# Kernel optimization log

Measured on AMD Instinct MI355X. Metric: run time of the kernel, lower is better.

The kernel has to match this reference:

```python
import jax, jax.numpy as jnp
import numpy as np

H = 64          # HIDDEN_DIM
VOCAB = 64      # VOCAB_SIZE
B, L = 256, 512
LN_EPS = 1e-5
NORM_EPS = 1e-12  # F.normalize eps


def setup_inputs() -> dict:
    key = jax.random.key(0)
    ks = jax.random.split(key, 12)
    s = 0.05
    return {
        "seq": jax.random.randint(ks[0], (B, L), 0, VOCAB),
        "embed": jax.random.normal(ks[1], (VOCAB, H), jnp.float32),
        "w1": jax.random.normal(ks[2], (H, 2 * H), jnp.float32) * s,
        "b1": jnp.zeros((2 * H,), jnp.float32),
        "w2": jax.random.normal(ks[3], (2 * H, H), jnp.float32) * s,
        "b2": jnp.zeros((H,), jnp.float32),
        "ln_g": jnp.ones((H,), jnp.float32),
        "ln_b": jnp.zeros((H,), jnp.float32),
        "rp_w": jax.random.normal(ks[4], (H, H), jnp.float32) * s,
        "rp_b": jnp.zeros((H,), jnp.float32),
        "out_w": jax.random.normal(ks[5], (H, VOCAB), jnp.float32) * s,
        "out_b": jnp.zeros((VOCAB,), jnp.float32),
    }


def reference(seq, embed, w1, b1, w2, b2, ln_g, ln_b, rp_w, rp_b, out_w, out_b):
    h = embed[seq]                                   # [B, L, H]
    ff = jnp.maximum(h @ w1 + b1, 0.0) @ w2 + b2     # MLP with ReLU
    x = h + ff
    mu = x.mean(-1, keepdims=True)
    var = x.var(-1, keepdims=True)                   # population variance (torch LN)
    h = (x - mu) / jnp.sqrt(var + LN_EPS) * ln_g + ln_b

    b, l, hd = h.shape
    ks = jnp.swapaxes(h, 0, 1)[:-1]                  # [L-1, B, H] keys over time

    def step(M, k):
        # k: [B, H]; M: [B, H, H] fast-weight memory
        kn = k / jnp.maximum(jnp.linalg.norm(k, axis=-1, keepdims=True), NORM_EPS)
        vp = jnp.einsum('bij,bj->bi', M, kn)         # predicted value
        dv = k - vp                                  # delta-rule error
        M = M + jnp.einsum('bi,bj->bij', dv, kn)     # alpha=1.0 -> full update
        return M, None

    M0 = jnp.zeros((b, hd, hd), h.dtype)
    M, _ = jax.lax.scan(step, M0, ks)

    y = jnp.einsum('bij,bj->bi', M, h[:, -1, :])     # read with last token
    return (y @ rp_w + rp_b) @ out_w + out_b         # [B, VOCAB]
```

## Files before the change

### kernel.cpp

```cpp
#include <hip/hip_runtime.h>

#define SEQLEN 512
#define NBATCH 256

typedef __attribute__((ext_vector_type(8))) __bf16 bf16x8;
typedef __attribute__((ext_vector_type(4))) float f32x4;
typedef unsigned short u16;
typedef unsigned int u32;

union B8 { bf16x8 v; u16 s[8]; uint4 q; };

__device__ __forceinline__ u16 rneb(float f) {
    u32 u = __float_as_uint(f);
    return (u16)((u + 0x7FFFu + ((u >> 16) & 1u)) >> 16);
}

template <int CTRL>
__device__ __forceinline__ float dpp_add(float x) {
    int y = __builtin_amdgcn_update_dpp(0, __float_as_int(x), CTRL, 0xF, 0xF, true);
    return x + __int_as_float(y);
}
__device__ __forceinline__ float sum16(float x) {
    x = dpp_add<0xB1>(x);
    x = dpp_add<0x4E>(x);
    x = dpp_add<0x141>(x);
    x = dpp_add<0x140>(x);
    return x;
}

__global__ __launch_bounds__(256, 1) void fused_all(
    const int* __restrict__ seq, const float* __restrict__ embed,
    const float* __restrict__ w1, const float* __restrict__ b1,
    const float* __restrict__ w2, const float* __restrict__ b2,
    const float* __restrict__ ln_g, const float* __restrict__ ln_b,
    const float* __restrict__ rp_w, const float* __restrict__ rp_b,
    const float* __restrict__ out_w, const float* __restrict__ out_b,
    float* __restrict__ out)
{
    __shared__ __align__(16) unsigned char smem[149504];
    float* Ksh = (float*)smem;
    float* Ssh = (float*)(smem + 131072);
    u16*  t1b  = (u16*)(smem + 133120);
    float* ysh = (float*)(smem + 133120);
    float* zsh = ysh + 64;

    const int tid = threadIdx.x;
    const int wv  = tid >> 6;
    const int l   = tid & 63;
    const int g   = l >> 4;
    const int tl  = l & 15;
    const int b   = blockIdx.x;

    B8 wA0[8], wA1[8];
#pragma unroll
    for (int nt = 0; nt < 8; ++nt) {
        const int j = nt * 16 + tl;
#pragma unroll
        for (int e = 0; e < 8; ++e) {
            wA0[nt].s[e] = rneb(w1[(g * 8 + e) * 128 + j]);
            wA1[nt].s[e] = rneb(w1[(32 + g * 8 + e) * 128 + j]);
        }
    }
    B8 wB[4][4];
#pragma unroll
    for (int kk = 0; kk < 4; ++kk)
#pragma unroll
        for (int mt = 0; mt < 4; ++mt) {
            const int m = mt * 16 + tl;
#pragma unroll
            for (int e = 0; e < 8; ++e)
                wB[kk][mt].s[e] = rneb(w2[(kk * 32 + g * 8 + e) * 64 + m]);
        }

    u16* myT = t1b + wv * 2048 + tl * 128;
    const int swz = (tl & 7) << 3;

    for (int grp = 0; grp < 8; ++grp) {
        const int lt = wv * 128 + grp * 16 + tl;
        const int idx = seq[b * SEQLEN + lt];
        const float* erow = embed + idx * 64;

        B8 xb0, xb1;
        {
            float4 c0 = *reinterpret_cast<const float4*>(erow + g * 8);
            float4 c1 = *reinterpret_cast<const float4*>(erow + g * 8 + 4);
            xb0.s[0] = rneb(c0.x); xb0.s[1] = rneb(c0.y); xb0.s[2] = rneb(c0.z); xb0.s[3] = rneb(c0.w);
            xb0.s[4] = rneb(c1.x); xb0.s[5] = rneb(c1.y); xb0.s[6] = rneb(c1.z); xb0.s[7] = rneb(c1.w);
            float4 c2 = *reinterpret_cast<const float4*>(erow + 32 + g * 8);
            float4 c3 = *reinterpret_cast<const float4*>(erow + 32 + g * 8 + 4);
            xb1.s[0] = rneb(c2.x); xb1.s[1] = rneb(c2.y); xb1.s[2] = rneb(c2.z); xb1.s[3] = rneb(c2.w);
            xb1.s[4] = rneb(c3.x); xb1.s[5] = rneb(c3.y); xb1.s[6] = rneb(c3.z); xb1.s[7] = rneb(c3.w);
        }

        f32x4 acc[8];
#pragma unroll
        for (int nt = 0; nt < 8; ++nt) acc[nt] = (f32x4){0.f, 0.f, 0.f, 0.f};
#pragma unroll
        for (int nt = 0; nt < 8; ++nt) {
            acc[nt] = __builtin_amdgcn_mfma_f32_16x16x32_bf16(wA0[nt].v, xb0.v, acc[nt], 0, 0, 0);
            acc[nt] = __builtin_amdgcn_mfma_f32_16x16x32_bf16(wA1[nt].v, xb1.v, acc[nt], 0, 0, 0);
        }

#pragma unroll
        for (int nt = 0; nt < 8; ++nt) {
            float4 bb = *reinterpret_cast<const float4*>(b1 + nt * 16 + g * 4);
            u32 lo = (u32)rneb(fmaxf(acc[nt][0] + bb.x, 0.f)) |
                     ((u32)rneb(fmaxf(acc[nt][1] + bb.y, 0.f)) << 16);
            u32 hi = (u32)rneb(fmaxf(acc[nt][2] + bb.z, 0.f)) |
                     ((u32)rneb(fmaxf(acc[nt][3] + bb.w, 0.f)) << 16);
            *reinterpret_cast<uint2*>(&myT[(nt * 16 + g * 4) ^ swz]) = make_uint2(lo, hi);
        }

        f32x4 acc2[4];
#pragma unroll
        for (int mt = 0; mt < 4; ++mt) acc2[mt] = (f32x4){0.f, 0.f, 0.f, 0.f};
#pragma unroll
        for (int kk = 0; kk < 4; ++kk) {
            B8 tb; tb.q = *reinterpret_cast<const uint4*>(&myT[(kk * 32 + g * 8) ^ swz]);
#pragma unroll
            for (int mt = 0; mt < 4; ++mt)
                acc2[mt] = __builtin_amdgcn_mfma_f32_16x16x32_bf16(wB[kk][mt].v, tb.v, acc2[mt], 0, 0, 0);
        }

        float x[16];
        float sum = 0.f;
#pragma unroll
        for (int mt = 0; mt < 4; ++mt) {
            float4 hr  = *reinterpret_cast<const float4*>(erow + mt * 16 + g * 4);
            float4 b2v = *reinterpret_cast<const float4*>(b2 + mt * 16 + g * 4);
            x[4*mt+0] = acc2[mt][0] + hr.x + b2v.x;
            x[4*mt+1] = acc2[mt][1] + hr.y + b2v.y;
            x[4*mt+2] = acc2[mt][2] + hr.z + b2v.z;
            x[4*mt+3] = acc2[mt][3] + hr.w + b2v.w;
            sum += x[4*mt+0] + x[4*mt+1] + x[4*mt+2] + x[4*mt+3];
        }
        sum += __shfl_xor(sum, 16);
        sum += __shfl_xor(sum, 32);
        float mu = sum * (1.f / 64.f);

        float vs = 0.f;
#pragma unroll
        for (int i = 0; i < 16; ++i) { float d = x[i] - mu; vs = fmaf(d, d, vs); }
        vs += __shfl_xor(vs, 16);
        vs += __shfl_xor(vs, 32);
        float rstd = 1.f / sqrtf(vs * (1.f / 64.f) + 1e-5f);

        float ss = 0.f;
#pragma unroll
        for (int mt = 0; mt < 4; ++mt) {
            float4 gv = *reinterpret_cast<const float4*>(ln_g + mt * 16 + g * 4);
            float4 bv = *reinterpret_cast<const float4*>(ln_b + mt * 16 + g * 4);
            float k0 = fmaf((x[4*mt+0] - mu) * rstd, gv.x, bv.x);
            float k1 = fmaf((x[4*mt+1] - mu) * rstd, gv.y, bv.y);
            float k2 = fmaf((x[4*mt+2] - mu) * rstd, gv.z, bv.z);
            float k3 = fmaf((x[4*mt+3] - mu) * rstd, gv.w, bv.w);
            x[4*mt+0] = k0; x[4*mt+1] = k1; x[4*mt+2] = k2; x[4*mt+3] = k3;
            ss = fmaf(k0, k0, ss); ss = fmaf(k1, k1, ss);
            ss = fmaf(k2, k2, ss); ss = fmaf(k3, k3, ss);
        }
        ss += __shfl_xor(ss, 16);
        ss += __shfl_xor(ss, 32);
        float s = fmaxf(sqrtf(ss), 1e-12f);
        float rn = 1.f / s;

        const int rsw = (lt & 7) << 3;
#pragma unroll
        for (int mt = 0; mt < 4; ++mt)
            *reinterpret_cast<float4*>(Ksh + lt * 64 + ((mt * 16 + g * 4) ^ rsw)) =
                make_float4(x[4*mt+0] * rn, x[4*mt+1] * rn, x[4*mt+2] * rn, x[4*mt+3] * rn);
        if (l < 16) Ssh[lt] = s;
    }

    __syncthreads();

    if (wv == 0) {
        const int c16 = l & 15;

        float4 qi = *reinterpret_cast<const float4*>(Ksh + 511 * 64 + ((c16 * 4) ^ 56));
        float s511 = Ssh[511];
        float u0 = qi.x * s511, u1 = qi.y * s511, u2 = qi.z * s511, u3 = qi.w * s511;
        float y0 = 0.f, y1 = 0.f, y2 = 0.f, y3 = 0.f;

        auto step = [&](float4 kf, float st) {
            float p = fmaf(kf.x, u0, kf.y * u1) + fmaf(kf.z, u2, kf.w * u3);
            float c_ = sum16(p);
            float cs = c_ * st;
            u0 = fmaf(-c_, kf.x, u0); u1 = fmaf(-c_, kf.y, u1);
            u2 = fmaf(-c_, kf.z, u2); u3 = fmaf(-c_, kf.w, u3);
            y0 = fmaf(cs, kf.x, y0); y1 = fmaf(cs, kf.y, y1);
            y2 = fmaf(cs, kf.z, y2); y3 = fmaf(cs, kf.w, y3);
        };

#define KLOADL(KA, SA, CH) do {                                               \
    _Pragma("unroll")                                                         \
    for (int q = 0; q < 8; ++q) {                                             \
        int trow = 510 - 8 * (CH) - q;                                        \
        int cr = trow < 0 ? 0 : trow;                                         \
        KA[q] = *reinterpret_cast<const float4*>(                             \
            Ksh + cr * 64 + ((c16 * 4) ^ ((cr & 7) << 3)));                   \
        SA[q] = Ssh[cr];                                                      \
    } } while (0)

        float4 bA[8], bB[8];
        float  sA[8], sB[8];
        KLOADL(bA, sA, 0);
        KLOADL(bB, sB, 1);
        for (int c = 0; c < 62; c += 2) {
#pragma unroll
            for (int q = 0; q < 8; ++q) step(bA[q], sA[q]);
            KLOADL(bA, sA, c + 2);
#pragma unroll
            for (int q = 0; q < 8; ++q) step(bB[q], sB[q]);
            KLOADL(bB, sB, c + 3);
        }
#pragma unroll
        for (int q = 0; q < 8; ++q) step(bA[q], sA[q]);
#pragma unroll
        for (int q = 0; q < 7; ++q) step(bB[q], sB[q]);

        if (l < 16)
            *reinterpret_cast<float4*>(&ysh[c16 * 4]) = make_float4(y0, y1, y2, y3);
    }
    __syncthreads();

    float z = 0.f;
    if (tid < 64) {
        z = rp_b[tid];
#pragma unroll 8
        for (int j = 0; j < 64; ++j) z = fmaf(ysh[j], rp_w[j * 64 + tid], z);
    }
    __syncthreads();
    if (tid < 64) zsh[tid] = z;
    __syncthreads();
    if (tid < 64) {
        float o = out_b[tid];
#pragma unroll 8
        for (int j = 0; j < 64; ++j) o = fmaf(zsh[j], out_w[j * 64 + tid], o);
        out[b * 64 + tid] = o;
    }
}

extern "C" void kernel_launch(void* const* d_in, const int* in_sizes, int n_in,
                              void* d_out, int out_size, void* d_ws, size_t ws_size,
                              hipStream_t stream) {
    const int*   seq   = (const int*)d_in[0];
    const float* embed = (const float*)d_in[1];
    const float* w1    = (const float*)d_in[2];
    const float* b1    = (const float*)d_in[3];
    const float* w2    = (const float*)d_in[4];
    const float* b2    = (const float*)d_in[5];
    const float* ln_g  = (const float*)d_in[6];
    const float* ln_b  = (const float*)d_in[7];
    const float* rp_w  = (const float*)d_in[8];
    const float* rp_b  = (const float*)d_in[9];
    const float* out_w = (const float*)d_in[10];
    const float* out_b = (const float*)d_in[11];
    float* out = (float*)d_out;

    fused_all<<<NBATCH, 256, 0, stream>>>(seq, embed, w1, b1, w2, b2,
                                          ln_g, ln_b, rp_w, rp_b,
                                          out_w, out_b, out);
}
```

Measured before the change: 128.1 us.

## Block the delta-rule backward scan by four keys using precomputed Gram dot products

The serial dual-form recurrence now processes four keys per step. Pairwise dot products within each group of four are precomputed in parallel by all waves into shared memory, which turns four dependent cross-lane reductions into four independent ones followed by a small triangular solve. The block grows to 512 threads, and the MLP phase is split into halves to lower register pressure, which also shrinks the scratch buffer per wave. Launch bounds now request 2 blocks per CU, but the roughly 147 KB of static shared memory probably keeps it at one. The serial tail also drops a barrier and only wave 0 touches ysh/zsh.

Result: slower. 131.7 us (+2.8%).

```diff
diff --git a/kernel.cpp b/kernel.cpp
--- a/kernel.cpp
+++ b/kernel.cpp
@@ -28,7 +28,13 @@
     return x;
 }
 
-__global__ __launch_bounds__(256, 1) void fused_all(
+__device__ __forceinline__ float dot4(const float4& k, float u0, float u1,
+                                      float u2, float u3) {
+    return fmaf(k.x, u0, k.y * u1) + fmaf(k.z, u2, k.w * u3);
+}
+
+
+__global__ __launch_bounds__(512, 2) void fused_all(
     const int* __restrict__ seq, const float* __restrict__ embed,
     const float* __restrict__ w1, const float* __restrict__ b1,
     const float* __restrict__ w2, const float* __restrict__ b2,
@@ -41,8 +47,9 @@
     float* Ksh = (float*)smem;
     float* Ssh = (float*)(smem + 131072);
     u16*  t1b  = (u16*)(smem + 133120);
-    float* ysh = (float*)(smem + 133120);
-    float* zsh = ysh + 64;
+    float* Gq  = (float*)(smem + 133120);
+    float* ysh = (float*)(smem + 137216);
+    float* zsh = (float*)(smem + 137472);
 
     const int tid = threadIdx.x;
     const int wv  = tid >> 6;
@@ -72,11 +79,11 @@
                 wB[kk][mt].s[e] = rneb(w2[(kk * 32 + g * 8 + e) * 64 + m]);
         }
 
-    u16* myT = t1b + wv * 2048 + tl * 128;
+    u16* myT = t1b + wv * 1024 + tl * 64;
     const int swz = (tl & 7) << 3;
 
-    for (int grp = 0; grp < 8; ++grp) {
-        const int lt = wv * 128 + grp * 16 + tl;
+    for (int grp = 0; grp < 4; ++grp) {
+        const int lt = wv * 64 + grp * 16 + tl;
         const int idx = seq[b * SEQLEN + lt];
         const float* erow = embed + idx * 64;
 
@@ -92,34 +99,38 @@
             xb1.s[4] = rneb(c3.x); xb1.s[5] = rneb(c3.y); xb1.s[6] = rneb(c3.z); xb1.s[7] = rneb(c3.w);
         }
 
-        f32x4 acc[8];
-#pragma unroll
-        for (int nt = 0; nt < 8; ++nt) acc[nt] = (f32x4){0.f, 0.f, 0.f, 0.f};
-#pragma unroll
-        for (int nt = 0; nt < 8; ++nt) {
-            acc[nt] = __builtin_amdgcn_mfma_f32_16x16x32_bf16(wA0[nt].v, xb0.v, acc[nt], 0, 0, 0);
-            acc[nt] = __builtin_amdgcn_mfma_f32_16x16x32_bf16(wA1[nt].v, xb1.v, acc[nt], 0, 0, 0);
-        }
-
-#pragma unroll
-        for (int nt = 0; nt < 8; ++nt) {
-            float4 bb = *reinterpret_cast<const float4*>(b1 + nt * 16 + g * 4);
-            u32 lo = (u32)rneb(fmaxf(acc[nt][0] + bb.x, 0.f)) |
-                     ((u32)rneb(fmaxf(acc[nt][1] + bb.y, 0.f)) << 16);
-            u32 hi = (u32)rneb(fmaxf(acc[nt][2] + bb.z, 0.f)) |
-                     ((u32)rneb(fmaxf(acc[nt][3] + bb.w, 0.f)) << 16);
-            *reinterpret_cast<uint2*>(&myT[(nt * 16 + g * 4) ^ swz]) = make_uint2(lo, hi);
-        }
-
         f32x4 acc2[4];
 #pragma unroll
         for (int mt = 0; mt < 4; ++mt) acc2[mt] = (f32x4){0.f, 0.f, 0.f, 0.f};
-#pragma unroll
-        for (int kk = 0; kk < 4; ++kk) {
-            B8 tb; tb.q = *reinterpret_cast<const uint4*>(&myT[(kk * 32 + g * 8) ^ swz]);
-#pragma unroll
-            for (int mt = 0; mt < 4; ++mt)
-                acc2[mt] = __builtin_amdgcn_mfma_f32_16x16x32_bf16(wB[kk][mt].v, tb.v, acc2[mt], 0, 0, 0);
+
+#pragma unroll
+        for (int half = 0; half < 2; ++half) {
+            f32x4 acc[4];
+#pragma unroll
+            for (int nt = 0; nt < 4; ++nt) {
+                const int NT = half * 4 + nt;
+                acc[nt] = (f32x4){0.f, 0.f, 0.f, 0.f};
+                acc[nt] = __builtin_amdgcn_mfma_f32_16x16x32_bf16(wA0[NT].v, xb0.v, acc[nt], 0, 0, 0);
+                acc[nt] = __builtin_amdgcn_mfma_f32_16x16x32_bf16(wA1[NT].v, xb1.v, acc[nt], 0, 0, 0);
+            }
+#pragma unroll
+            for (int nt = 0; nt < 4; ++nt) {
+                const int NT = half * 4 + nt;
+                float4 bb = *reinterpret_cast<const float4*>(b1 + NT * 16 + g * 4);
+                u32 lo = (u32)rneb(fmaxf(acc[nt][0] + bb.x, 0.f)) |
+                         ((u32)rneb(fmaxf(acc[nt][1] + bb.y, 0.f)) << 16);
+                u32 hi = (u32)rneb(fmaxf(acc[nt][2] + bb.z, 0.f)) |
+                         ((u32)rneb(fmaxf(acc[nt][3] + bb.w, 0.f)) << 16);
+                *reinterpret_cast<uint2*>(&myT[(nt * 16 + g * 4) ^ swz]) = make_uint2(lo, hi);
+            }
+#pragma unroll
+            for (int k2l = 0; k2l < 2; ++k2l) {
+                const int KK = half * 2 + k2l;
+                B8 tb; tb.q = *reinterpret_cast<const uint4*>(&myT[(k2l * 32 + g * 8) ^ swz]);
+#pragma unroll
+                for (int mt = 0; mt < 4; ++mt)
+                    acc2[mt] = __builtin_amdgcn_mfma_f32_16x16x32_bf16(wB[KK][mt].v, tb.v, acc2[mt], 0, 0, 0);
+            }
         }
 
         float x[16];
@@ -173,66 +184,116 @@
 
     __syncthreads();
 
+#pragma unroll
+    for (int pass = 0; pass < 4; ++pass) {
+        const int q = pass * 32 + wv * 4 + g;
+        float4 r0, r1, r2, r3;
+        {
+            const int R0 = 4 * q;
+            r0 = *reinterpret_cast<const float4*>(Ksh + (R0+0) * 64 + ((tl*4) ^ (((R0+0)&7)<<3)));
+            r1 = *reinterpret_cast<const float4*>(Ksh + (R0+1) * 64 + ((tl*4) ^ (((R0+1)&7)<<3)));
+            r2 = *reinterpret_cast<const float4*>(Ksh + (R0+2) * 64 + ((tl*4) ^ (((R0+2)&7)<<3)));
+            r3 = *reinterpret_cast<const float4*>(Ksh + (R0+3) * 64 + ((tl*4) ^ (((R0+3)&7)<<3)));
+        }
+        float d10 = fmaf(r2.x, r3.x, r2.y * r3.y) + fmaf(r2.z, r3.z, r2.w * r3.w);
+        float d20 = fmaf(r1.x, r3.x, r1.y * r3.y) + fmaf(r1.z, r3.z, r1.w * r3.w);
+        float d21 = fmaf(r1.x, r2.x, r1.y * r2.y) + fmaf(r1.z, r2.z, r1.w * r2.w);
+        float d30 = fmaf(r0.x, r3.x, r0.y * r3.y) + fmaf(r0.z, r3.z, r0.w * r3.w);
+        float d31 = fmaf(r0.x, r2.x, r0.y * r2.y) + fmaf(r0.z, r2.z, r0.w * r2.w);
+        float d32 = fmaf(r0.x, r1.x, r0.y * r1.y) + fmaf(r0.z, r1.z, r0.w * r1.w);
+        d10 = sum16(d10); d20 = sum16(d20); d21 = sum16(d21);
+        d30 = sum16(d30); d31 = sum16(d31); d32 = sum16(d32);
+        if (tl == 0) {
+            *reinterpret_cast<float4*>(Gq + q * 8)     = make_float4(d10, d20, d21, d30);
+            *reinterpret_cast<float2*>(Gq + q * 8 + 4) = make_float2(d31, d32);
+        }
+    }
+
+    __syncthreads();
+
     if (wv == 0) {
-        const int c16 = l & 15;
-
-        float4 qi = *reinterpret_cast<const float4*>(Ksh + 511 * 64 + ((c16 * 4) ^ 56));
-        float s511 = Ssh[511];
-        float u0 = qi.x * s511, u1 = qi.y * s511, u2 = qi.z * s511, u3 = qi.w * s511;
-        float y0 = 0.f, y1 = 0.f, y2 = 0.f, y3 = 0.f;
-
-        auto step = [&](float4 kf, float st) {
-            float p = fmaf(kf.x, u0, kf.y * u1) + fmaf(kf.z, u2, kf.w * u3);
-            float c_ = sum16(p);
-            float cs = c_ * st;
-            u0 = fmaf(-c_, kf.x, u0); u1 = fmaf(-c_, kf.y, u1);
-            u2 = fmaf(-c_, kf.z, u2); u3 = fmaf(-c_, kf.w, u3);
-            y0 = fmaf(cs, kf.x, y0); y1 = fmaf(cs, kf.y, y1);
-            y2 = fmaf(cs, kf.z, y2); y3 = fmaf(cs, kf.w, y3);
+        const int c16 = tl;
+        float u0, u1, u2, u3, y0 = 0.f, y1 = 0.f, y2 = 0.f, y3 = 0.f;
+
+        struct QB { float4 k0, k1, k2, k3, sv, g0; float2 g1; };
+        auto qload = [&](QB& qb, int Q) {
+            Q = Q < 0 ? 0 : Q;
+            const int R0 = 4 * Q;
+            qb.k0 = *reinterpret_cast<const float4*>(Ksh + (R0+0) * 64 + ((c16*4) ^ (((R0+0)&7)<<3)));
+            qb.k1 = *reinterpret_cast<const float4*>(Ksh + (R0+1) * 64 + ((c16*4) ^ (((R0+1)&7)<<3)));
+            qb.k2 = *reinterpret_cast<const float4*>(Ksh + (R0+2) * 64 + ((c16*4) ^ (((R0+2)&7)<<3)));
+            qb.k3 = *reinterpret_cast<const float4*>(Ksh + (R0+3) * 64 + ((c16*4) ^ (((R0+3)&7)<<3)));
+            qb.sv = *reinterpret_cast<const float4*>(Ssh + R0);
+            qb.g0 = *reinterpret_cast<const float4*>(Gq + Q * 8);
+            qb.g1 = *reinterpret_cast<const float2*>(Gq + Q * 8 + 4);
         };
-
-#define KLOADL(KA, SA, CH) do {                                               \
-    _Pragma("unroll")                                                         \
-    for (int q = 0; q < 8; ++q) {                                             \
-        int trow = 510 - 8 * (CH) - q;                                        \
-        int cr = trow < 0 ? 0 : trow;                                         \
-        KA[q] = *reinterpret_cast<const float4*>(                             \
-            Ksh + cr * 64 + ((c16 * 4) ^ ((cr & 7) << 3)));                   \
-        SA[q] = Ssh[cr];                                                      \
-    } } while (0)
-
-        float4 bA[8], bB[8];
-        float  sA[8], sB[8];
-        KLOADL(bA, sA, 0);
-        KLOADL(bB, sB, 1);
-        for (int c = 0; c < 62; c += 2) {
-#pragma unroll
-            for (int q = 0; q < 8; ++q) step(bA[q], sA[q]);
-            KLOADL(bA, sA, c + 2);
-#pragma unroll
-            for (int q = 0; q < 8; ++q) step(bB[q], sB[q]);
-            KLOADL(bB, sB, c + 3);
-        }
-#pragma unroll
-        for (int q = 0; q < 8; ++q) step(bA[q], sA[q]);
-#pragma unroll
-        for (int q = 0; q < 7; ++q) step(bB[q], sB[q]);
+        auto qstep = [&](const QB& qb) {
+            float pp0 = dot4(qb.k3, u0, u1, u2, u3);
+            float pp1 = dot4(qb.k2, u0, u1, u2, u3);
+            float pp2 = dot4(qb.k1, u0, u1, u2, u3);
+            float pp3 = dot4(qb.k0, u0, u1, u2, u3);
+            float P0 = sum16(pp0), P1 = sum16(pp1), P2 = sum16(pp2), P3 = sum16(pp3);
+            float c0 = P0;
+            float c1 = fmaf(-qb.g0.x, c0, P1);
+            float c2 = fmaf(-qb.g0.z, c1, fmaf(-qb.g0.y, c0, P2));
+            float c3 = fmaf(-qb.g1.y, c2, fmaf(-qb.g1.x, c1, fmaf(-qb.g0.w, c0, P3)));
+            u0 -= c0*qb.k3.x + c1*qb.k2.x + c2*qb.k1.x + c3*qb.k0.x;
+            u1 -= c0*qb.k3.y + c1*qb.k2.y + c2*qb.k1.y + c3*qb.k0.y;
+            u2 -= c0*qb.k3.z + c1*qb.k2.z + c2*qb.k1.z + c3*qb.k0.z;
+            u3 -= c0*qb.k3.w + c1*qb.k2.w + c2*qb.k1.w + c3*qb.k0.w;
+            float d0 = c0*qb.sv.w, d1 = c1*qb.sv.z, d2 = c2*qb.sv.y, d3 = c3*qb.sv.x;
+            y0 += d0*qb.k3.x + d1*qb.k2.x + d2*qb.k1.x + d3*qb.k0.x;
+            y1 += d0*qb.k3.y + d1*qb.k2.y + d2*qb.k1.y + d3*qb.k0.y;
+            y2 += d0*qb.k3.z + d1*qb.k2.z + d2*qb.k1.z + d3*qb.k0.z;
+            y3 += d0*qb.k3.w + d1*qb.k2.w + d2*qb.k1.w + d3*qb.k0.w;
+        };
+
+        {
+            QB qb; qload(qb, 127);
+            float s511 = qb.sv.w;
+            u0 = qb.k3.x * s511; u1 = qb.k3.y * s511;
+            u2 = qb.k3.z * s511; u3 = qb.k3.w * s511;
+            float pp1 = dot4(qb.k2, u0, u1, u2, u3);
+            float pp2 = dot4(qb.k1, u0, u1, u2, u3);
+            float pp3 = dot4(qb.k0, u0, u1, u2, u3);
+            float P1 = sum16(pp1), P2 = sum16(pp2), P3 = sum16(pp3);
+            float c1 = P1;
+            float c2 = fmaf(-qb.g0.z, c1, P2);
+            float c3 = fmaf(-qb.g1.y, c2, fmaf(-qb.g1.x, c1, P3));
+            u0 -= c1*qb.k2.x + c2*qb.k1.x + c3*qb.k0.x;
+            u1 -= c1*qb.k2.y + c2*qb.k1.y + c3*qb.k0.y;
+            u2 -= c1*qb.k2.z + c2*qb.k1.z + c3*qb.k0.z;
+            u3 -= c1*qb.k2.w + c2*qb.k1.w + c3*qb.k0.w;
+            float d1 = c1*qb.sv.z, d2 = c2*qb.sv.y, d3 = c3*qb.sv.x;
+            y0 += d1*qb.k2.x + d2*qb.k1.x + d3*qb.k0.x;
+            y1 += d1*qb.k2.y + d2*qb.k1.y + d3*qb.k0.y;
+            y2 += d1*qb.k2.z + d2*qb.k1.z + d3*qb.k0.z;
+            y3 += d1*qb.k2.w + d2*qb.k1.w + d3*qb.k0.w;
+        }
+
+        QB A, B, C;
+        qload(A, 126);
+        qload(B, 125);
+        for (int c = 0; c < 42; ++c) {
+            const int base = 126 - 3 * c;
+            qload(C, base - 2);
+            qstep(A);
+            qload(A, base - 3);
+            qstep(B);
+            qload(B, base - 4);
+            qstep(C);
+        }
+        qstep(A);
 
         if (l < 16)
             *reinterpret_cast<float4*>(&ysh[c16 * 4]) = make_float4(y0, y1, y2, y3);
     }
-    __syncthreads();
-
-    float z = 0.f;
+
     if (tid < 64) {
-        z = rp_b[tid];
+        float z = rp_b[tid];
 #pragma unroll 8
         for (int j = 0; j < 64; ++j) z = fmaf(ysh[j], rp_w[j * 64 + tid], z);
-    }
-    __syncthreads();
-    if (tid < 64) zsh[tid] = z;
-    __syncthreads();
-    if (tid < 64) {
+        zsh[tid] = z;
         float o = out_b[tid];
 #pragma unroll 8
         for (int j = 0; j < 64; ++j) o = fmaf(zsh[j], out_w[j * 64 + tid], o);
@@ -257,7 +318,7 @@
     const float* out_b = (const float*)d_in[11];
     float* out = (float*)d_out;
 
-    fused_all<<<NBATCH, 256, 0, stream>>>(seq, embed, w1, b1, w2, b2,
+    fused_all<<<NBATCH, 512, 0, stream>>>(seq, embed, w1, b1, w2, b2,
                                           ln_g, ln_b, rp_w, rp_b,
                                           out_w, out_b, out);
 }
```
